# Kernel tuning notes

Measured on AMD Instinct MI355X. Metric: run time of the kernel, lower is better.

## Reference

```python
import jax, jax.numpy as jnp
import numpy as np

N, E, DIN, DH, DOUT = 50000, 800000, 128, 256, 128
EPS = 1e-5
SLOPE = 0.01  # torch leaky_relu default


def setup_inputs() -> dict:
    key = jax.random.key(0)
    ks = jax.random.split(key, 8)
    w = lambda k, shape: jax.random.normal(k, shape, jnp.float32) * 0.05
    return {
        "x": jax.random.normal(ks[0], (N, DIN), jnp.float32),
        "edge_index": jax.random.randint(ks[1], (2, E), 0, N, jnp.int32),
        "W0": w(ks[2], (DH, DIN)),  "b0": jnp.zeros((DH,), jnp.float32),
        "g0": jnp.ones((DH,), jnp.float32), "be0": jnp.zeros((DH,), jnp.float32),
        "W1": w(ks[3], (DH, DH)),   "b1": jnp.zeros((DH,), jnp.float32),
        "g1": jnp.ones((DH,), jnp.float32), "be1": jnp.zeros((DH,), jnp.float32),
        "W2": w(ks[4], (DOUT, DH)), "b2": jnp.zeros((DOUT,), jnp.float32),
        "g2": jnp.ones((DOUT,), jnp.float32), "be2": jnp.zeros((DOUT,), jnp.float32),
    }


def _gcn_forward(x, edge_index, params):
    n = x.shape[0]
    loop = jnp.arange(n, dtype=edge_index.dtype)
    src = jnp.concatenate([edge_index[0], loop])  # add self-loops
    dst = jnp.concatenate([edge_index[1], loop])
    deg = jnp.zeros((n,), x.dtype).at[dst].add(1.0)
    dinv = jax.lax.rsqrt(deg)  # deg >= 1 due to self-loops
    enorm = (dinv[src] * dinv[dst])[:, None]  # [E+N, 1]

    def conv(h, W, b):
        h = h @ W.T  # linear first (PyG GCNConv), messages in out_dim
        msg = h[src] * enorm
        return jax.ops.segment_sum(msg, dst, num_segments=n) + b

    def bn(h, g, be):  # BatchNorm1d, training-mode batch stats (biased var)
        mu = h.mean(0)
        var = ((h - mu) ** 2).mean(0)
        return (h - mu) * jax.lax.rsqrt(var + EPS) * g + be

    (W0, b0, g0, be0, W1, b1, g1, be1, W2, b2, g2, be2) = params
    h = jax.nn.leaky_relu(bn(conv(x, W0, b0), g0, be0), SLOPE)
    h = jax.nn.leaky_relu(bn(conv(h, W1, b1), g1, be1), SLOPE)
    h = bn(conv(h, W2, b2), g2, be2)  # last layer: no leaky_relu
    return h


def reference(x, edge_index, W0, b0, g0, be0, W1, b1, g1, be1, W2, b2, g2, be2):
    return _gcn_forward(x, edge_index,
                        (W0, b0, g0, be0, W1, b1, g1, be1, W2, b2, g2, be2))
```

## Files before the change

kernel.cpp:

```cpp
#include <hip/hip_runtime.h>
#include <hip/hip_bf16.h>

#define N_NODES 50000
#define N_EDGES 800000
#define DIN 128
#define DH   256
#define DOUT 128
#define EPSV 1e-5f
#define SLOPE 0.01f
#define SCAN_NB ((N_NODES + 255) / 256)

typedef __bf16 bf16x8 __attribute__((ext_vector_type(8)));
typedef __bf16 bf16x4 __attribute__((ext_vector_type(4)));
typedef float  f32x4  __attribute__((ext_vector_type(4)));

__global__ void cast_kernel(const float* __restrict__ src, __bf16* __restrict__ dst, int n4) {
    int i = blockIdx.x * blockDim.x + threadIdx.x;
    if (i < n4) {
        float4 v = ((const float4*)src)[i];
        bf16x4 o; o[0] = (__bf16)v.x; o[1] = (__bf16)v.y; o[2] = (__bf16)v.z; o[3] = (__bf16)v.w;
        ((bf16x4*)dst)[i] = o;
    }
}

__global__ void cast_scale_kernel(const float* __restrict__ src, const float* __restrict__ dinv,
                                  __bf16* __restrict__ dst) {
    int i = blockIdx.x * blockDim.x + threadIdx.x;
    if (i < N_NODES * DIN / 8) {
        int row = i / (DIN / 8);
        float d = dinv[row];
        float4 a = ((const float4*)src)[i * 2];
        float4 b = ((const float4*)src)[i * 2 + 1];
        bf16x8 o;
        o[0] = (__bf16)(a.x * d); o[1] = (__bf16)(a.y * d);
        o[2] = (__bf16)(a.z * d); o[3] = (__bf16)(a.w * d);
        o[4] = (__bf16)(b.x * d); o[5] = (__bf16)(b.y * d);
        o[6] = (__bf16)(b.z * d); o[7] = (__bf16)(b.w * d);
        ((bf16x8*)dst)[i] = o;
    }
}

__global__ void deg_kernel(const int* __restrict__ dst, int* __restrict__ deg) {
    int i = blockIdx.x * blockDim.x + threadIdx.x;
    if (i < N_EDGES) atomicAdd(&deg[dst[i]], 1);
}

__global__ void dinv_kernel(const int* __restrict__ deg, float* __restrict__ dinv) {
    int i = blockIdx.x * blockDim.x + threadIdx.x;
    if (i < N_NODES) dinv[i] = rsqrtf((float)deg[i] + 1.0f);
}

__global__ __launch_bounds__(256) void scan_bsum(const int* __restrict__ deg,
                                                 int* __restrict__ bsum) {
    __shared__ int lds[256];
    int i = blockIdx.x * 256 + threadIdx.x;
    lds[threadIdx.x] = (i < N_NODES) ? deg[i] + 1 : 0;
    __syncthreads();
    #pragma unroll
    for (int off = 128; off > 0; off >>= 1) {
        if (threadIdx.x < off) lds[threadIdx.x] += lds[threadIdx.x + off];
        __syncthreads();
    }
    if (threadIdx.x == 0) bsum[blockIdx.x] = lds[0];
}

__global__ __launch_bounds__(256) void scan_boffs(const int* __restrict__ bsum,
                                                  int* __restrict__ boffs) {
    __shared__ int lds[256];
    const int t = threadIdx.x;
    lds[t] = (t < SCAN_NB) ? bsum[t] : 0;
    __syncthreads();
    #pragma unroll
    for (int off = 1; off < 256; off <<= 1) {
        int add = (t >= off) ? lds[t - off] : 0;
        __syncthreads();
        lds[t] += add;
        __syncthreads();
    }
    boffs[t] = (t == 0) ? 0 : lds[t - 1];
}

__global__ __launch_bounds__(256) void scan_write(const int* __restrict__ deg,
                                                  const int* __restrict__ boffs,
                                                  int* __restrict__ rp) {
    __shared__ int lds[256];
    const int t = threadIdx.x;
    int i = blockIdx.x * 256 + t;
    int v = (i < N_NODES) ? deg[i] + 1 : 0;
    lds[t] = v;
    __syncthreads();
    #pragma unroll
    for (int off = 1; off < 256; off <<= 1) {
        int add = (t >= off) ? lds[t - off] : 0;
        __syncthreads();
        lds[t] += add;
        __syncthreads();
    }
    if (i < N_NODES) rp[i] = boffs[blockIdx.x] + lds[t] - v;
    if (i == N_NODES - 1) rp[N_NODES] = boffs[blockIdx.x] + lds[t];
}

__global__ void scatter_kernel(const int* __restrict__ ei,
                               const int* __restrict__ rp, int* __restrict__ cursor,
                               int* __restrict__ csr) {
    int e = blockIdx.x * blockDim.x + threadIdx.x;
    if (e >= N_EDGES + N_NODES) return;
    int pos, src;
    if (e < N_EDGES) {
        src = ei[e]; int dst = ei[N_EDGES + e];
        pos = rp[dst] + atomicAdd(&cursor[dst], 1);
    } else {
        src = e - N_EDGES;
        pos = rp[src + 1] - 1;
    }
    csr[pos] = src;
}

template<int C8, bool OUTF32>
__global__ __launch_bounds__(256) void spmm_b(const int* __restrict__ rp,
                                              const int* __restrict__ csr,
                                              const float* __restrict__ dinv,
                                              const __bf16* __restrict__ h,
                                              void* __restrict__ outp) {
    constexpr int C = C8 * 8;
    constexpr int RPB = 256 / C8;
    const int r = blockIdx.x * RPB + threadIdx.x / C8;
    const int l = threadIdx.x % C8;
    if (r >= N_NODES) return;
    const bf16x8* __restrict__ h8 = (const bf16x8*)h;
    const int e0 = rp[r], e1 = rp[r + 1];
    float acc0[8] = {}, acc1[8] = {};
    int e = e0;
    for (; e + 8 <= e1; e += 8) {
        int p[8];
        #pragma unroll
        for (int u = 0; u < 8; ++u) p[u] = csr[e + u];
        bf16x8 v[8];
        #pragma unroll
        for (int u = 0; u < 8; ++u) v[u] = h8[(long)p[u] * C8 + l];
        #pragma unroll
        for (int u = 0; u < 8; ++u) {
            #pragma unroll
            for (int j = 0; j < 8; ++j) {
                if (u & 1) acc1[j] += (float)v[u][j];
                else       acc0[j] += (float)v[u][j];
            }
        }
    }
    for (; e + 2 <= e1; e += 2) {
        int p0 = csr[e], p1 = csr[e + 1];
        bf16x8 v0 = h8[(long)p0 * C8 + l];
        bf16x8 v1 = h8[(long)p1 * C8 + l];
        #pragma unroll
        for (int j = 0; j < 8; ++j) {
            acc0[j] += (float)v0[j];
            acc1[j] += (float)v1[j];
        }
    }
    if (e < e1) {
        int p0 = csr[e];
        bf16x8 v0 = h8[(long)p0 * C8 + l];
        #pragma unroll
        for (int j = 0; j < 8; ++j) acc0[j] += (float)v0[j];
    }
    const float d = dinv[r];
    float res[8];
    #pragma unroll
    for (int j = 0; j < 8; ++j) res[j] = (acc0[j] + acc1[j]) * d;
    if (OUTF32) {
        float* o = (float*)outp + (long)r * C + l * 8;
        ((float4*)o)[0] = make_float4(res[0], res[1], res[2], res[3]);
        ((float4*)o)[1] = make_float4(res[4], res[5], res[6], res[7]);
    } else {
        bf16x8 ob;
        #pragma unroll
        for (int j = 0; j < 8; ++j) ob[j] = (__bf16)res[j];
        ((bf16x8*)outp)[(long)r * C8 + l] = ob;
    }
}

template<int K, int NC, bool FUSE_BN, bool RELU, bool SCALE>
__global__ __launch_bounds__(256) void gemm_tile(const __bf16* __restrict__ A,
                                                 const __bf16* __restrict__ W,
                                                 const float* __restrict__ ss,
                                                 const float* __restrict__ dinv,
                                                 __bf16* __restrict__ C,
                                                 int M) {
    constexpr int NW = NC / 64;
    constexpr int MW = 4 / NW;
    constexpr int BM = MW * 64;
    constexpr int NSTEP = K / 32;
    __shared__ __bf16 As[2][BM][40];

    const int tid = threadIdx.x;
    const int wave = tid >> 6, lane = tid & 63;
    const int ln15 = lane & 15, kg = lane >> 4;
    const int wm = wave / NW, wn = wave % NW;
    const int m0 = blockIdx.x * BM;
    const int srow = tid >> 2, schunk = tid & 3;

    int grow[MW];
    #pragma unroll
    for (int p = 0; p < MW; ++p) {
        int gr = m0 + p * 64 + srow;
        grow[p] = gr < M ? gr : M - 1;
    }

    f32x4 acc[4][4];
    #pragma unroll
    for (int i = 0; i < 4; ++i)
        #pragma unroll
        for (int j = 0; j < 4; ++j) acc[i][j] = (f32x4){0.f, 0.f, 0.f, 0.f};

#define LOAD_A(vv, kt_)                                                         \
    _Pragma("unroll")                                                           \
    for (int p = 0; p < MW; ++p)                                                \
        vv[p] = *(const bf16x8*)(A + (long)grow[p] * K + (kt_) + schunk * 8);

#define XFORM_A(vv, kt_)                                                        \
    if (FUSE_BN) {                                                              \
        const f32x4* ss4 = (const f32x4*)ss;                                    \
        int ci = ((kt_) + schunk * 8) >> 2;                                     \
        f32x4 sc0 = ss4[ci],            sc1 = ss4[ci + 1];                      \
        f32x4 sh0 = ss4[(K >> 2) + ci], sh1 = ss4[(K >> 2) + ci + 1];           \
        _Pragma("unroll")                                                       \
        for (int p = 0; p < MW; ++p) {                                          \
            float f[8];                                                         \
            _Pragma("unroll")                                                   \
            for (int j = 0; j < 4; ++j) {                                       \
                f[j]     = fmaf((float)vv[p][j],     sc0[j], sh0[j]);           \
                f[j + 4] = fmaf((float)vv[p][j + 4], sc1[j], sh1[j]);           \
            }                                                                   \
            if (RELU) {                                                         \
                _Pragma("unroll")                                               \
                for (int j = 0; j < 8; ++j) f[j] = f[j] > 0.f ? f[j] : SLOPE * f[j]; \
            }                                                                   \
            _Pragma("unroll")                                                   \
            for (int j = 0; j < 8; ++j) vv[p][j] = (__bf16)f[j];                \
        }                                                                       \
    }

#define WRITE_A(buf, vv)                                                        \
    _Pragma("unroll")                                                           \
    for (int p = 0; p < MW; ++p)                                                \
        *(bf16x8*)(&As[buf][p * 64 + srow][schunk * 8]) = vv[p];

    bf16x8 v0[MW], v[MW];
    LOAD_A(v0, 0)
    XFORM_A(v0, 0)
    WRITE_A(0, v0)
    if (NSTEP > 1) {
        LOAD_A(v, 32)
        XFORM_A(v, 32)
    }
    __syncthreads();

    int cur = 0;
    #pragma unroll
    for (int step = 0; step < NSTEP; ++step) {
        const int kt = step * 32;
        if (step + 1 < NSTEP) {
            WRITE_A(cur ^ 1, v)
        }
        bf16x8 vn[MW];
        if (step + 2 < NSTEP) {
            LOAD_A(vn, kt + 64)
        }
        bf16x8 b[4];
        #pragma unroll
        for (int j = 0; j < 4; ++j)
            b[j] = *(const bf16x8*)(W + (long)(wn * 64 + j * 16 + ln15) * K + kt + kg * 8);
        #pragma unroll
        for (int i = 0; i < 4; ++i) {
            bf16x8 a = *(const bf16x8*)(&As[cur][wm * 64 + i * 16 + ln15][kg * 8]);
            #pragma unroll
            for (int j = 0; j < 4; ++j)
                acc[i][j] = __builtin_amdgcn_mfma_f32_16x16x32_bf16(a, b[j], acc[i][j], 0, 0, 0);
        }
        if (step + 2 < NSTEP) {
            XFORM_A(vn, kt + 64)
            #pragma unroll
            for (int p = 0; p < MW; ++p) v[p] = vn[p];
        }
        __syncthreads();
        cur ^= 1;
    }
#undef LOAD_A
#undef XFORM_A
#undef WRITE_A

    #pragma unroll
    for (int i = 0; i < 4; ++i) {
        #pragma unroll
        for (int q = 0; q < 4; ++q) {
            int r = m0 + wm * 64 + i * 16 + kg * 4 + q;
            if (r < M) {
                float d = SCALE ? dinv[r] : 1.0f;
                #pragma unroll
                for (int j = 0; j < 4; ++j)
                    C[(long)r * NC + wn * 64 + j * 16 + ln15] = (__bf16)(acc[i][j][q] * d);
            }
        }
    }
}

#define NB_STATS 128
template<int C, bool BF16>
__global__ __launch_bounds__(256) void bn_stats(const void* __restrict__ hp,
                                                float* __restrict__ partial) {
    constexpr int LPR = C / 4;
    constexpr int RPI = 256 / LPR;
    const int chunk = threadIdx.x % LPR;
    const int rof   = threadIdx.x / LPR;
    float s[4] = {}, s2[4] = {};
    for (int r = blockIdx.x * RPI + rof; r < N_NODES; r += NB_STATS * RPI) {
        float v[4];
        if (BF16) {
            bf16x4 x = ((const bf16x4*)hp)[(long)r * LPR + chunk];
            #pragma unroll
            for (int j = 0; j < 4; ++j) v[j] = (float)x[j];
        } else {
            float4 x = ((const float4*)hp)[(long)r * LPR + chunk];
            v[0] = x.x; v[1] = x.y; v[2] = x.z; v[3] = x.w;
        }
        #pragma unroll
        for (int j = 0; j < 4; ++j) { s[j] += v[j]; s2[j] += v[j] * v[j]; }
    }
    __shared__ float red[256 * 8];
    #pragma unroll
    for (int j = 0; j < 4; ++j) { red[threadIdx.x * 8 + j] = s[j]; red[threadIdx.x * 8 + 4 + j] = s2[j]; }
    __syncthreads();
    if (rof == 0) {
        #pragma unroll
        for (int g = 1; g < RPI; ++g) {
            #pragma unroll
            for (int j = 0; j < 4; ++j) {
                s[j]  += red[(g * LPR + chunk) * 8 + j];
                s2[j] += red[(g * LPR + chunk) * 8 + 4 + j];
            }
        }
        #pragma unroll
        for (int j = 0; j < 4; ++j) {
            partial[blockIdx.x * 2 * C + chunk * 4 + j]     = s[j];
            partial[blockIdx.x * 2 * C + C + chunk * 4 + j] = s2[j];
        }
    }
}

template<int C>
__global__ void bn_reduce(const float* __restrict__ partial, const float* __restrict__ g,
                          const float* __restrict__ be, float* __restrict__ ss) {
    int c = threadIdx.x;
    float s_0 = 0.f, s_1 = 0.f, q_0 = 0.f, q_1 = 0.f;
    #pragma unroll 4
    for (int b = 0; b < NB_STATS; b += 2) {
        s_0 += partial[b * 2 * C + c];
        q_0 += partial[b * 2 * C + C + c];
        s_1 += partial[(b + 1) * 2 * C + c];
        q_1 += partial[(b + 1) * 2 * C + C + c];
    }
    float s = s_0 + s_1, s2 = q_0 + q_1;
    const float invn = 1.0f / (float)N_NODES;
    float mean = s * invn;
    float var  = s2 * invn - mean * mean;
    float rstd = rsqrtf(var + EPSV);
    float sc = g[c] * rstd;
    ss[c] = sc;
    ss[C + c] = be[c] - mean * sc;
}

template<int C>
__global__ __launch_bounds__(256) void bn_apply_f32(float* __restrict__ h,
                                                    const float* __restrict__ ss) {
    constexpr int LPR = C / 4;
    const long total = (long)N_NODES * LPR;
    const long stride = (long)gridDim.x * blockDim.x;
    for (long idx = (long)blockIdx.x * blockDim.x + threadIdx.x; idx < total; idx += stride) {
        int chunk = (int)(idx % LPR);
        float4 sc = ((const float4*)ss)[chunk];
        float4 sh = ((const float4*)(ss + C))[chunk];
        float4 x = ((float4*)h)[idx];
        x.x = fmaf(x.x, sc.x, sh.x); x.y = fmaf(x.y, sc.y, sh.y);
        x.z = fmaf(x.z, sc.z, sh.z); x.w = fmaf(x.w, sc.w, sh.w);
        ((float4*)h)[idx] = x;
    }
}

extern "C" void kernel_launch(void* const* d_in, const int* in_sizes, int n_in,
                              void* d_out, int out_size, void* d_ws, size_t ws_size,
                              hipStream_t stream) {
    const float* x   = (const float*)d_in[0];
    const int*   ei  = (const int*)  d_in[1];
    const float* W0  = (const float*)d_in[2];
    const float* g0  = (const float*)d_in[4];
    const float* be0 = (const float*)d_in[5];
    const float* W1  = (const float*)d_in[6];
    const float* g1  = (const float*)d_in[8];
    const float* be1 = (const float*)d_in[9];
    const float* W2  = (const float*)d_in[10];
    const float* g2  = (const float*)d_in[12];
    const float* be2 = (const float*)d_in[13];
    float* out = (float*)d_out;

    char* wsb = (char*)d_ws;
    auto alloc = [&](size_t bytes) { char* p = wsb; wsb += (bytes + 255) & ~255UL; return p; };
    int*    deg     = (int*)   alloc(N_NODES * 4);
    int*    rp      = (int*)   alloc((N_NODES + 4) * 4);
    int*    cursor  = (int*)   alloc(N_NODES * 4);
    float*  dinv    = (float*) alloc(N_NODES * 4);
    int*    bsum    = (int*)   alloc(256 * 4);
    int*    boffs   = (int*)   alloc(257 * 4);
    float*  partial = (float*) alloc(NB_STATS * 2 * DH * 4);
    float*  ss      = (float*) alloc(2 * DH * 4);
    int*    csr     = (int*)   alloc((size_t)(N_EDGES + N_NODES) * 4);
    __bf16* w0b     = (__bf16*)alloc(DH * DIN * 2);
    __bf16* w1b     = (__bf16*)alloc(DH * DH * 2);
    __bf16* w2b     = (__bf16*)alloc(DOUT * DH * 2);
    __bf16* xb      = (__bf16*)alloc((size_t)N_NODES * DIN * 2);
    __bf16* bf0     = (__bf16*)alloc((size_t)N_NODES * DH * 2);
    __bf16* bf1     = (__bf16*)alloc((size_t)N_NODES * DH * 2);

    cast_kernel<<<(DH * DIN / 4 + 255) / 256, 256, 0, stream>>>(W0, w0b, DH * DIN / 4);
    cast_kernel<<<(DH * DH  / 4 + 255) / 256, 256, 0, stream>>>(W1, w1b, DH * DH / 4);
    cast_kernel<<<(DOUT * DH / 4 + 255) / 256, 256, 0, stream>>>(W2, w2b, DOUT * DH / 4);

    hipMemsetAsync(deg, 0, N_NODES * 4, stream);
    hipMemsetAsync(cursor, 0, N_NODES * 4, stream);
    deg_kernel<<<(N_EDGES + 255) / 256, 256, 0, stream>>>(ei + N_EDGES, deg);
    dinv_kernel<<<(N_NODES + 255) / 256, 256, 0, stream>>>(deg, dinv);
    scan_bsum<<<SCAN_NB, 256, 0, stream>>>(deg, bsum);
    scan_boffs<<<1, 256, 0, stream>>>(bsum, boffs);
    scan_write<<<SCAN_NB, 256, 0, stream>>>(deg, boffs, rp);
    scatter_kernel<<<(N_EDGES + N_NODES + 255) / 256, 256, 0, stream>>>(ei, rp, cursor, csr);

    cast_scale_kernel<<<(N_NODES * (DIN / 8) + 255) / 256, 256, 0, stream>>>(x, dinv, xb);

    spmm_b<DIN / 8, false><<<(N_NODES * (DIN / 8) + 255) / 256, 256, 0, stream>>>(
        rp, csr, dinv, xb, bf0);
    gemm_tile<DIN, DH, false, false, false><<<(N_NODES + 63) / 64, 256, 0, stream>>>(
        bf0, w0b, nullptr, nullptr, bf1, N_NODES);
    bn_stats<DH, true><<<NB_STATS, 256, 0, stream>>>(bf1, partial);
    bn_reduce<DH><<<1, DH, 0, stream>>>(partial, g0, be0, ss);

    gemm_tile<DH, DH, true, true, true><<<(N_NODES + 63) / 64, 256, 0, stream>>>(
        bf1, w1b, ss, dinv, bf0, N_NODES);
    spmm_b<DH / 8, false><<<(N_NODES * (DH / 8) + 255) / 256, 256, 0, stream>>>(
        rp, csr, dinv, bf0, bf1);
    bn_stats<DH, true><<<NB_STATS, 256, 0, stream>>>(bf1, partial);
    bn_reduce<DH><<<1, DH, 0, stream>>>(partial, g1, be1, ss);

    gemm_tile<DH, DOUT, true, true, true><<<(N_NODES + 127) / 128, 256, 0, stream>>>(
        bf1, w2b, ss, dinv, bf0, N_NODES);
    spmm_b<DOUT / 8, true><<<(N_NODES * (DOUT / 8) + 255) / 256, 256, 0, stream>>>(
        rp, csr, dinv, bf0, out);
    bn_stats<DOUT, false><<<NB_STATS, 256, 0, stream>>>(out, partial);
    bn_reduce<DOUT><<<1, DOUT, 0, stream>>>(partial, g2, be2, ss);
    bn_apply_f32<DOUT><<<2048, 256, 0, stream>>>(out, ss);
}
```

Measured before the change: 400.0 us.

## Fuse launches, BN stats into first GEMM, and bf16 final SpMM output

Merges the three weight casts into one kernel, folds dinv computation into the scan block-sum kernel, and merges the two memsets into one. The first GEMM epilogue now accumulates per-column BN partial sums, removing one bn_stats pass. CSR indices use nontemporal stores and loads. The last SpMM writes bf16 instead of fp32, and a new apply kernel converts to fp32 output, which lowers precision of the final pre-BN values and makes bn_reduce sum many more partials serially.

```diff
diff --git a/kernel.cpp b/kernel.cpp
--- a/kernel.cpp
+++ b/kernel.cpp
@@ -14,19 +14,26 @@
 typedef __bf16 bf16x4 __attribute__((ext_vector_type(4)));
 typedef float  f32x4  __attribute__((ext_vector_type(4)));
 
-__global__ void cast_kernel(const float* __restrict__ src, __bf16* __restrict__ dst, int n4) {
+__global__ void cast3_kernel(const float* __restrict__ W0, const float* __restrict__ W1,
+                             const float* __restrict__ W2,
+                             __bf16* __restrict__ w0b, __bf16* __restrict__ w1b,
+                             __bf16* __restrict__ w2b) {
+    constexpr int n0 = DH * DIN / 4, n1 = DH * DH / 4, n2 = DOUT * DH / 4;
     int i = blockIdx.x * blockDim.x + threadIdx.x;
-    if (i < n4) {
-        float4 v = ((const float4*)src)[i];
-        bf16x4 o; o[0] = (__bf16)v.x; o[1] = (__bf16)v.y; o[2] = (__bf16)v.z; o[3] = (__bf16)v.w;
-        ((bf16x4*)dst)[i] = o;
-    }
+    const float* src; __bf16* dst; int k;
+    if (i < n0)           { src = W0; dst = w0b; k = i; }
+    else if (i < n0 + n1) { src = W1; dst = w1b; k = i - n0; }
+    else if (i < n0 + n1 + n2) { src = W2; dst = w2b; k = i - n0 - n1; }
+    else return;
+    float4 v = ((const float4*)src)[k];
+    bf16x4 o; o[0] = (__bf16)v.x; o[1] = (__bf16)v.y; o[2] = (__bf16)v.z; o[3] = (__bf16)v.w;
+    ((bf16x4*)dst)[k] = o;
 }
 
 __global__ void cast_scale_kernel(const float* __restrict__ src, const float* __restrict__ dinv,
                                   __bf16* __restrict__ dst) {
     int i = blockIdx.x * blockDim.x + threadIdx.x;
-    if (i < N_NODES * DIN / 8) {
+    if (i < N_NODES * (DIN / 8)) {
         int row = i / (DIN / 8);
         float d = dinv[row];
         float4 a = ((const float4*)src)[i * 2];
@@ -45,16 +52,17 @@
     if (i < N_EDGES) atomicAdd(&deg[dst[i]], 1);
 }
 
-__global__ void dinv_kernel(const int* __restrict__ deg, float* __restrict__ dinv) {
-    int i = blockIdx.x * blockDim.x + threadIdx.x;
-    if (i < N_NODES) dinv[i] = rsqrtf((float)deg[i] + 1.0f);
-}
-
 __global__ __launch_bounds__(256) void scan_bsum(const int* __restrict__ deg,
-                                                 int* __restrict__ bsum) {
+                                                 int* __restrict__ bsum,
+                                                 float* __restrict__ dinv) {
     __shared__ int lds[256];
     int i = blockIdx.x * 256 + threadIdx.x;
-    lds[threadIdx.x] = (i < N_NODES) ? deg[i] + 1 : 0;
+    int dv = 0;
+    if (i < N_NODES) {
+        dv = deg[i] + 1;
+        dinv[i] = rsqrtf((float)dv);
+    }
+    lds[threadIdx.x] = dv;
     __syncthreads();
     #pragma unroll
     for (int off = 128; off > 0; off >>= 1) {
@@ -113,16 +121,15 @@
         src = e - N_EDGES;
         pos = rp[src + 1] - 1;
     }
-    csr[pos] = src;
-}
-
-template<int C8, bool OUTF32>
+    __builtin_nontemporal_store(src, &csr[pos]);
+}
+
+template<int C8>
 __global__ __launch_bounds__(256) void spmm_b(const int* __restrict__ rp,
                                               const int* __restrict__ csr,
                                               const float* __restrict__ dinv,
                                               const __bf16* __restrict__ h,
-                                              void* __restrict__ outp) {
-    constexpr int C = C8 * 8;
+                                              __bf16* __restrict__ outp) {
     constexpr int RPB = 256 / C8;
     const int r = blockIdx.x * RPB + threadIdx.x / C8;
     const int l = threadIdx.x % C8;
@@ -134,7 +141,7 @@
     for (; e + 8 <= e1; e += 8) {
         int p[8];
         #pragma unroll
-        for (int u = 0; u < 8; ++u) p[u] = csr[e + u];
+        for (int u = 0; u < 8; ++u) p[u] = __builtin_nontemporal_load(csr + e + u);
         bf16x8 v[8];
         #pragma unroll
         for (int u = 0; u < 8; ++u) v[u] = h8[(long)p[u] * C8 + l];
@@ -148,7 +155,8 @@
         }
     }
     for (; e + 2 <= e1; e += 2) {
-        int p0 = csr[e], p1 = csr[e + 1];
+        int p0 = __builtin_nontemporal_load(csr + e);
+        int p1 = __builtin_nontemporal_load(csr + e + 1);
         bf16x8 v0 = h8[(long)p0 * C8 + l];
         bf16x8 v1 = h8[(long)p1 * C8 + l];
         #pragma unroll
@@ -158,33 +166,25 @@
         }
     }
     if (e < e1) {
-        int p0 = csr[e];
+        int p0 = __builtin_nontemporal_load(csr + e);
         bf16x8 v0 = h8[(long)p0 * C8 + l];
         #pragma unroll
         for (int j = 0; j < 8; ++j) acc0[j] += (float)v0[j];
     }
     const float d = dinv[r];
-    float res[8];
-    #pragma unroll
-    for (int j = 0; j < 8; ++j) res[j] = (acc0[j] + acc1[j]) * d;
-    if (OUTF32) {
-        float* o = (float*)outp + (long)r * C + l * 8;
-        ((float4*)o)[0] = make_float4(res[0], res[1], res[2], res[3]);
-        ((float4*)o)[1] = make_float4(res[4], res[5], res[6], res[7]);
-    } else {
-        bf16x8 ob;
-        #pragma unroll
-        for (int j = 0; j < 8; ++j) ob[j] = (__bf16)res[j];
-        ((bf16x8*)outp)[(long)r * C8 + l] = ob;
-    }
-}
-
-template<int K, int NC, bool FUSE_BN, bool RELU, bool SCALE>
+    bf16x8 ob;
+    #pragma unroll
+    for (int j = 0; j < 8; ++j) ob[j] = (__bf16)((acc0[j] + acc1[j]) * d);
+    ((bf16x8*)outp)[(long)r * C8 + l] = ob;
+}
+
+template<int K, int NC, bool FUSE_BN, bool RELU, bool SCALE, bool FUSE_STATS>
 __global__ __launch_bounds__(256) void gemm_tile(const __bf16* __restrict__ A,
                                                  const __bf16* __restrict__ W,
                                                  const float* __restrict__ ss,
                                                  const float* __restrict__ dinv,
                                                  __bf16* __restrict__ C,
+                                                 float* __restrict__ partial,
                                                  int M) {
     constexpr int NW = NC / 64;
     constexpr int MW = 4 / NW;
@@ -289,24 +289,50 @@
 #undef XFORM_A
 #undef WRITE_A
 
+    float sst[4] = {}, qst[4] = {};
     #pragma unroll
     for (int i = 0; i < 4; ++i) {
         #pragma unroll
         for (int q = 0; q < 4; ++q) {
             int r = m0 + wm * 64 + i * 16 + kg * 4 + q;
-            if (r < M) {
-                float d = SCALE ? dinv[r] : 1.0f;
-                #pragma unroll
-                for (int j = 0; j < 4; ++j)
-                    C[(long)r * NC + wn * 64 + j * 16 + ln15] = (__bf16)(acc[i][j][q] * d);
+            bool ok = r < M;
+            int rc = ok ? r : 0;
+            float d = SCALE ? dinv[rc] : 1.0f;
+            #pragma unroll
+            for (int j = 0; j < 4; ++j) {
+                __bf16 bv = (__bf16)(acc[i][j][q] * d);
+                if (ok) {
+                    C[(long)r * NC + wn * 64 + j * 16 + ln15] = bv;
+                    if (FUSE_STATS) {
+                        float fv = (float)bv;
+                        sst[j] += fv; qst[j] += fv * fv;
+                    }
+                }
             }
         }
     }
+    if (FUSE_STATS) {
+        #pragma unroll
+        for (int j = 0; j < 4; ++j) {
+            sst[j] += __shfl_xor(sst[j], 16, 64);
+            sst[j] += __shfl_xor(sst[j], 32, 64);
+            qst[j] += __shfl_xor(qst[j], 16, 64);
+            qst[j] += __shfl_xor(qst[j], 32, 64);
+        }
+        if (kg == 0) {
+            #pragma unroll
+            for (int j = 0; j < 4; ++j) {
+                int col = wn * 64 + j * 16 + ln15;
+                partial[(long)blockIdx.x * (2 * NC) + col]      = sst[j];
+                partial[(long)blockIdx.x * (2 * NC) + NC + col] = qst[j];
+            }
+        }
+    }
 }
 
 #define NB_STATS 128
-template<int C, bool BF16>
-__global__ __launch_bounds__(256) void bn_stats(const void* __restrict__ hp,
+template<int C>
+__global__ __launch_bounds__(256) void bn_stats(const __bf16* __restrict__ hp,
                                                 float* __restrict__ partial) {
     constexpr int LPR = C / 4;
     constexpr int RPI = 256 / LPR;
@@ -314,17 +340,12 @@
     const int rof   = threadIdx.x / LPR;
     float s[4] = {}, s2[4] = {};
     for (int r = blockIdx.x * RPI + rof; r < N_NODES; r += NB_STATS * RPI) {
-        float v[4];
-        if (BF16) {
-            bf16x4 x = ((const bf16x4*)hp)[(long)r * LPR + chunk];
-            #pragma unroll
-            for (int j = 0; j < 4; ++j) v[j] = (float)x[j];
-        } else {
-            float4 x = ((const float4*)hp)[(long)r * LPR + chunk];
-            v[0] = x.x; v[1] = x.y; v[2] = x.z; v[3] = x.w;
-        }
-        #pragma unroll
-        for (int j = 0; j < 4; ++j) { s[j] += v[j]; s2[j] += v[j] * v[j]; }
+        bf16x4 x = ((const bf16x4*)hp)[(long)r * LPR + chunk];
+        #pragma unroll
+        for (int j = 0; j < 4; ++j) {
+            float v = (float)x[j];
+            s[j] += v; s2[j] += v * v;
+        }
     }
     __shared__ float red[256 * 8];
     #pragma unroll
@@ -348,21 +369,19 @@
 }
 
 template<int C>
-__global__ void bn_reduce(const float* __restrict__ partial, const float* __restrict__ g,
-                          const float* __restrict__ be, float* __restrict__ ss) {
+__global__ void bn_reduce(const float* __restrict__ partial, int nb,
+                          const float* __restrict__ g, const float* __restrict__ be,
+                          float* __restrict__ ss) {
     int c = threadIdx.x;
-    float s_0 = 0.f, s_1 = 0.f, q_0 = 0.f, q_1 = 0.f;
+    float s = 0.f, q = 0.f;
     #pragma unroll 4
-    for (int b = 0; b < NB_STATS; b += 2) {
-        s_0 += partial[b * 2 * C + c];
-        q_0 += partial[b * 2 * C + C + c];
-        s_1 += partial[(b + 1) * 2 * C + c];
-        q_1 += partial[(b + 1) * 2 * C + C + c];
-    }
-    float s = s_0 + s_1, s2 = q_0 + q_1;
+    for (int b = 0; b < nb; ++b) {
+        s += partial[(long)b * 2 * C + c];
+        q += partial[(long)b * 2 * C + C + c];
+    }
     const float invn = 1.0f / (float)N_NODES;
     float mean = s * invn;
-    float var  = s2 * invn - mean * mean;
+    float var  = q * invn - mean * mean;
     float rstd = rsqrtf(var + EPSV);
     float sc = g[c] * rstd;
     ss[c] = sc;
@@ -370,7 +389,8 @@
 }
 
 template<int C>
-__global__ __launch_bounds__(256) void bn_apply_f32(float* __restrict__ h,
+__global__ __launch_bounds__(256) void bn_apply_b2f(const __bf16* __restrict__ in,
+                                                    float* __restrict__ outp,
                                                     const float* __restrict__ ss) {
     constexpr int LPR = C / 4;
     const long total = (long)N_NODES * LPR;
@@ -379,10 +399,13 @@
         int chunk = (int)(idx % LPR);
         float4 sc = ((const float4*)ss)[chunk];
         float4 sh = ((const float4*)(ss + C))[chunk];
-        float4 x = ((float4*)h)[idx];
-        x.x = fmaf(x.x, sc.x, sh.x); x.y = fmaf(x.y, sc.y, sh.y);
-        x.z = fmaf(x.z, sc.z, sh.z); x.w = fmaf(x.w, sc.w, sh.w);
-        ((float4*)h)[idx] = x;
+        bf16x4 x = ((const bf16x4*)in)[idx];
+        float4 o;
+        o.x = fmaf((float)x[0], sc.x, sh.x);
+        o.y = fmaf((float)x[1], sc.y, sh.y);
+        o.z = fmaf((float)x[2], sc.z, sh.z);
+        o.w = fmaf((float)x[3], sc.w, sh.w);
+        ((float4*)outp)[idx] = o;
     }
 }
 
@@ -402,15 +425,17 @@
     const float* be2 = (const float*)d_in[13];
     float* out = (float*)d_out;
 
+    const int GEMM0_NB = (N_NODES + 63) / 64;
+
     char* wsb = (char*)d_ws;
     auto alloc = [&](size_t bytes) { char* p = wsb; wsb += (bytes + 255) & ~255UL; return p; };
     int*    deg     = (int*)   alloc(N_NODES * 4);
+    int*    cursor  = (int*)   alloc(N_NODES * 4);
     int*    rp      = (int*)   alloc((N_NODES + 4) * 4);
-    int*    cursor  = (int*)   alloc(N_NODES * 4);
     float*  dinv    = (float*) alloc(N_NODES * 4);
     int*    bsum    = (int*)   alloc(256 * 4);
     int*    boffs   = (int*)   alloc(257 * 4);
-    float*  partial = (float*) alloc(NB_STATS * 2 * DH * 4);
+    float*  partial = (float*) alloc((size_t)GEMM0_NB * 2 * DH * 4);
     float*  ss      = (float*) alloc(2 * DH * 4);
     int*    csr     = (int*)   alloc((size_t)(N_EDGES + N_NODES) * 4);
     __bf16* w0b     = (__bf16*)alloc(DH * DIN * 2);
@@ -420,40 +445,37 @@
     __bf16* bf0     = (__bf16*)alloc((size_t)N_NODES * DH * 2);
     __bf16* bf1     = (__bf16*)alloc((size_t)N_NODES * DH * 2);
 
-    cast_kernel<<<(DH * DIN / 4 + 255) / 256, 256, 0, stream>>>(W0, w0b, DH * DIN / 4);
-    cast_kernel<<<(DH * DH  / 4 + 255) / 256, 256, 0, stream>>>(W1, w1b, DH * DH / 4);
-    cast_kernel<<<(DOUT * DH / 4 + 255) / 256, 256, 0, stream>>>(W2, w2b, DOUT * DH / 4);
-
-    hipMemsetAsync(deg, 0, N_NODES * 4, stream);
-    hipMemsetAsync(cursor, 0, N_NODES * 4, stream);
+    hipMemsetAsync(deg, 0, (size_t)((char*)cursor - (char*)deg) + N_NODES * 4, stream);
+
+    cast3_kernel<<<(DH * DIN / 4 + DH * DH / 4 + DOUT * DH / 4 + 255) / 256, 256, 0, stream>>>(
+        W0, W1, W2, w0b, w1b, w2b);
+
     deg_kernel<<<(N_EDGES + 255) / 256, 256, 0, stream>>>(ei + N_EDGES, deg);
-    dinv_kernel<<<(N_NODES + 255) / 256, 256, 0, stream>>>(deg, dinv);
-    scan_bsum<<<SCAN_NB, 256, 0, stream>>>(deg, bsum);
+    scan_bsum<<<SCAN_NB, 256, 0, stream>>>(deg, bsum, dinv);
     scan_boffs<<<1, 256, 0, stream>>>(bsum, boffs);
     scan_write<<<SCAN_NB, 256, 0, stream>>>(deg, boffs, rp);
     scatter_kernel<<<(N_EDGES + N_NODES + 255) / 256, 256, 0, stream>>>(ei, rp, cursor, csr);
 
     cast_scale_kernel<<<(N_NODES * (DIN / 8) + 255) / 256, 256, 0, stream>>>(x, dinv, xb);
 
-    spmm_b<DIN / 8, false><<<(N_NODES * (DIN / 8) + 255) / 256, 256, 0, stream>>>(
+    spmm_b<DIN / 8><<<(N_NODES * (DIN / 8) + 255) / 256, 256, 0, stream>>>(
         rp, csr, dinv, xb, bf0);
-    gemm_tile<DIN, DH, false, false, false><<<(N_NODES + 63) / 64, 256, 0, stream>>>(
-        bf0, w0b, nullptr, nullptr, bf1, N_NODES);
-    bn_stats<DH, true><<<NB_STATS, 256, 0, stream>>>(bf1, partial);
-    bn_reduce<DH><<<1, DH, 0, stream>>>(partial, g0, be0, ss);
-
-    gemm_tile<DH, DH, true, true, true><<<(N_NODES + 63) / 64, 256, 0, stream>>>(
-        bf1, w1b, ss, dinv, bf0, N_NODES);
-    spmm_b<DH / 8, false><<<(N_NODES * (DH / 8) + 255) / 256, 256, 0, stream>>>(
+    gemm_tile<DIN, DH, false, false, false, true><<<GEMM0_NB, 256, 0, stream>>>(
+        bf0, w0b, nullptr, nullptr, bf1, partial, N_NODES);
+    bn_reduce<DH><<<1, DH, 0, stream>>>(partial, GEMM0_NB, g0, be0, ss);
+
+    gemm_tile<DH, DH, true, true, true, false><<<(N_NODES + 63) / 64, 256, 0, stream>>>(
+        bf1, w1b, ss, dinv, bf0, nullptr, N_NODES);
+    spmm_b<DH / 8><<<(N_NODES * (DH / 8) + 255) / 256, 256, 0, stream>>>(
         rp, csr, dinv, bf0, bf1);
-    bn_stats<DH, true><<<NB_STATS, 256, 0, stream>>>(bf1, partial);
-    bn_reduce<DH><<<1, DH, 0, stream>>>(partial, g1, be1, ss);
-
-    gemm_tile<DH, DOUT, true, true, true><<<(N_NODES + 127) / 128, 256, 0, stream>>>(
-        bf1, w2b, ss, dinv, bf0, N_NODES);
-    spmm_b<DOUT / 8, true><<<(N_NODES * (DOUT / 8) + 255) / 256, 256, 0, stream>>>(
-        rp, csr, dinv, bf0, out);
-    bn_stats<DOUT, false><<<NB_STATS, 256, 0, stream>>>(out, partial);
-    bn_reduce<DOUT><<<1, DOUT, 0, stream>>>(partial, g2, be2, ss);
-    bn_apply_f32<DOUT><<<2048, 256, 0, stream>>>(out, ss);
-}
+    bn_stats<DH><<<NB_STATS, 256, 0, stream>>>(bf1, partial);
+    bn_reduce<DH><<<1, DH, 0, stream>>>(partial, NB_STATS, g1, be1, ss);
+
+    gemm_tile<DH, DOUT, true, true, true, false><<<(N_NODES + 127) / 128, 256, 0, stream>>>(
+        bf1, w2b, ss, dinv, bf0, nullptr, N_NODES);
+    spmm_b<DOUT / 8><<<(N_NODES * (DOUT / 8) + 255) / 256, 256, 0, stream>>>(
+        rp, csr, dinv, bf0, bf1);
+    bn_stats<DOUT><<<NB_STATS, 256, 0, stream>>>(bf1, partial);
+    bn_reduce<DOUT><<<1, DOUT, 0, stream>>>(partial, NB_STATS, g2, be2, ss);
+    bn_apply_b2f<DOUT><<<2048, 256, 0, stream>>>(bf1, out, ss);
+}
```

Result: slower. 458.5 us (+14.6%).
